# Performance work log

Measured on AMD Instinct MI355X. Metric: run time of the kernel, lower is better.

Reference implementation:

```python
import jax, jax.numpy as jnp
import numpy as np

B_, L_, H_, N_ = 8, 1024, 1024, 64

def setup_inputs() -> dict:
    key = jax.random.key(0)
    k1, k2, k3, k4 = jax.random.split(key, 4)
    return {
        "samples": jax.random.normal(k1, (B_, L_, 3 * H_), dtype=jnp.float32),
        "label_one_hot": jax.random.uniform(k2, (B_, L_, N_), dtype=jnp.float32),
        "predict": jax.random.normal(k3, (B_, L_, N_), dtype=jnp.float32),
        "W": jax.random.normal(k4, (H_, 3 * H_), dtype=jnp.float32) * (1.0 / np.sqrt(3 * H_)),
        "b_proj": jnp.zeros((H_,), dtype=jnp.float32),
    }

def reference(samples, label_one_hot, predict, W, b_proj):
    # projection: Linear(3H -> H)
    s = jnp.einsum("blk,hk->blh", samples, W) + b_proj          # [b,L,H]
    # dense similarity graph with diagonal masked out, row-softmax
    graph = jnp.einsum("blh,bmh->blm", s, s)                     # [b,L,L]
    L = graph.shape[1]
    eye = jnp.eye(L, dtype=graph.dtype)
    A = jax.nn.softmax(graph - 1e5 * eye, axis=-1)               # [b,L,L]
    # centered masked labels
    sup = label_one_hot
    row_has = (jnp.sum(sup, axis=-1) > 0.5).astype(sup.dtype)    # [b,L]
    total = jnp.sum(row_has, axis=-1)[:, None]                   # [b,1]
    avg = (jnp.sum(sup, axis=-2) / total)[:, None, :]            # [b,1,N]
    B0 = (sup - avg) * row_has[..., None]                        # [b,L,N]
    # diagonal inverse-degree scaling (elementwise, no dense diag matmul)
    d = 1.0 / (jnp.sum(A, axis=-1) + 1e-10)                      # [b,L]
    P = d[:, :, None] * jnp.swapaxes(A, -1, -2)                  # [b,L,L]
    Db = d[:, :, None] * B0                                      # [b,L,N]
    # 6-step power-iteration scan with residual injection at t==3
    ut = jnp.zeros_like(B0)
    for t in range(1, 7):
        ut = jnp.einsum("blm,bmn->bln", P, ut) + Db
        if t == 3:
            ut = ut + predict  # dropout is identity in eval mode
    return ut

if __name__ == "__main__":
    out = reference(**setup_inputs())
    print(out.shape, out.dtype)
```

## Files before the change

kernel.cpp:

```cpp
#include <hip/hip_runtime.h>


typedef _Float16 f16_t;
typedef f16_t f16x4 __attribute__((ext_vector_type(4)));
typedef f16_t f16x8 __attribute__((ext_vector_type(8)));
typedef float floatx4 __attribute__((ext_vector_type(4)));

__device__ __forceinline__ void async_copy16(const void* g, void* l) {
  __builtin_amdgcn_global_load_lds(
      (const __attribute__((address_space(1))) void*)g,
      (__attribute__((address_space(3))) void*)l, 16, 0, 0);
}

__device__ __forceinline__ f16_t hi_of(float x) { return (f16_t)x; }
__device__ __forceinline__ f16_t lo_of(float x, f16_t h) {
  return (f16_t)(x - (float)h);
}

__global__ __launch_bounds__(256) void prep_kernel(
    const float* __restrict__ W, f16_t* __restrict__ Whi, f16_t* __restrict__ Wlo,
    const float* __restrict__ samples, f16_t* __restrict__ SampH)
{
  const int bx = blockIdx.x, tid = threadIdx.x;
  if (bx < 3072) {
    const int i = bx * 256 + tid;
    float4 v = ((const float4*)W)[i];
    v.x *= 32.f; v.y *= 32.f; v.z *= 32.f; v.w *= 32.f;
    f16x4 h, l;
    f16_t h0 = hi_of(v.x); h[0] = h0; l[0] = lo_of(v.x, h0);
    f16_t h1 = hi_of(v.y); h[1] = h1; l[1] = lo_of(v.y, h1);
    f16_t h2 = hi_of(v.z); h[2] = h2; l[2] = lo_of(v.z, h2);
    f16_t h3 = hi_of(v.w); h[3] = h3; l[3] = lo_of(v.w, h3);
    *(f16x4*)(Whi + (size_t)i * 4) = h;
    *(f16x4*)(Wlo + (size_t)i * 4) = l;
  } else {
    const int i = (bx - 3072) * 256 + tid;
    const float4 v = ((const float4*)samples)[i];
    f16x4 h;
    h[0] = (f16_t)v.x; h[1] = (f16_t)v.y; h[2] = (f16_t)v.z; h[3] = (f16_t)v.w;
    *(f16x4*)(SampH + (size_t)i * 4) = h;
  }
}

struct Frags {
  f16x8 a[8];
  f16x8 bh0, bh1, bl0, bl1;
};

#define DSR(dst_, addr_, OFFSTR_) \
  asm volatile("ds_read_b128 %0, %1 offset:" OFFSTR_ : "=v"(dst_) : "v"(addr_))

__device__ __forceinline__ void read_frags_asm(unsigned sa, unsigned sb,
                                               Frags& f) {
  DSR(f.bh0, sb, "0");
  DSR(f.bh1, sb, "1024");
  DSR(f.bl0, sb, "8192");
  DSR(f.bl1, sb, "9216");
  DSR(f.a[0], sa, "0");
  DSR(f.a[1], sa, "1024");
  DSR(f.a[2], sa, "2048");
  DSR(f.a[3], sa, "3072");
  DSR(f.a[4], sa, "4096");
  DSR(f.a[5], sa, "5120");
  DSR(f.a[6], sa, "6144");
  DSR(f.a[7], sa, "7168");
}

__global__ __launch_bounds__(512, 2) void gemm1_pipe(
    const f16_t* __restrict__ Ag,
    const f16_t* __restrict__ BhG, const f16_t* __restrict__ BlG,
    const float* __restrict__ bias,
    f16_t* __restrict__ Chi, f16_t* __restrict__ Clo,
    int N, int K, float cscale)
{
  __shared__ __align__(16) char smem[131072];

  const int tid = threadIdx.x;
  const int lane = tid & 63;
  const int wave = tid >> 6;
  const int wm = wave >> 2;
  const int wn = wave & 3;
  const int bid0 = blockIdx.y * 8 + blockIdx.x;
  const int xk = bid0 & 7, xj = bid0 >> 3;
  const int m0 = ((xk >> 1) * 8 + (xj >> 2)) * 256;
  const int n0 = ((xk & 1) * 4 + (xj & 3)) * 128;
  const int fr = lane & 15;
  const int lch = lane >> 4;

  const int gA0 = tid;
  const int gA1 = tid + 512;
  const int rA0 = gA0 >> 2, lcA0 = (gA0 & 3) ^ ((rA0 >> 1) & 3);
  const int rA1 = gA1 >> 2, lcA1 = (gA1 & 3) ^ ((rA1 >> 1) & 3);
  const int rB = tid >> 2, lcB = (tid & 3) ^ ((rB >> 1) & 3);
  const f16_t* aSrc0 = Ag + (size_t)(m0 + rA0) * K + lcA0 * 8;
  const f16_t* aSrc1 = Ag + (size_t)(m0 + rA1) * K + lcA1 * 8;
  const f16_t* bhSrc = BhG + (size_t)(n0 + rB) * K + lcB * 8;
  const f16_t* blSrc = BlG + (size_t)(n0 + rB) * K + lcB * 8;
  char* ldsA0 = smem + gA0 * 16;
  char* ldsA1 = smem + gA1 * 16;
  char* ldsBh = smem + 16384 + (size_t)tid * 16;
  char* ldsBl = smem + 24576 + (size_t)tid * 16;

  const int swz = (lch ^ ((fr >> 1) & 3)) * 16;
  const int aoff = (wm * 128 + fr) * 64 + swz;
  const int boff = (wn * 32 + fr) * 64 + swz;
  const unsigned ldsBase =
      (unsigned)(size_t)(__attribute__((address_space(3))) char*)smem;
  const unsigned aA0 = ldsBase + (unsigned)aoff;
  const unsigned aA1 = aA0 + 32768u;
  const unsigned aA2 = aA0 + 65536u;
  const unsigned aA3 = aA0 + 98304u;
  const unsigned bA0 = ldsBase + 16384u + (unsigned)boff;
  const unsigned bA1 = bA0 + 32768u;
  const unsigned bA2 = bA0 + 65536u;
  const unsigned bA3 = bA0 + 98304u;

  floatx4 acc[8][2] = {};
  const int NS = K >> 5;

#define STAGE(SS_, SLOT_)                                     \
  do {                                                        \
    int ss = (SS_); if (ss >= NS) ss -= NS;                   \
    const int k0 = ss * 32;                                   \
    async_copy16(aSrc0 + k0, ldsA0 + (SLOT_) * 32768);        \
    async_copy16(aSrc1 + k0, ldsA1 + (SLOT_) * 32768);        \
    async_copy16(bhSrc + k0, ldsBh + (SLOT_) * 32768);        \
    async_copy16(blSrc + k0, ldsBl + (SLOT_) * 32768);        \
  } while (0)

#define MFMA8(F_, P_)                                                                                               \
  do {                                                                                                              \
    acc[2*(P_)][0]   = __builtin_amdgcn_mfma_f32_16x16x32_f16((F_).a[2*(P_)],   (F_).bh0, acc[2*(P_)][0],   0,0,0); \
    acc[2*(P_)][1]   = __builtin_amdgcn_mfma_f32_16x16x32_f16((F_).a[2*(P_)],   (F_).bh1, acc[2*(P_)][1],   0,0,0); \
    acc[2*(P_)+1][0] = __builtin_amdgcn_mfma_f32_16x16x32_f16((F_).a[2*(P_)+1], (F_).bh0, acc[2*(P_)+1][0], 0,0,0); \
    acc[2*(P_)+1][1] = __builtin_amdgcn_mfma_f32_16x16x32_f16((F_).a[2*(P_)+1], (F_).bh1, acc[2*(P_)+1][1], 0,0,0); \
    acc[2*(P_)][0]   = __builtin_amdgcn_mfma_f32_16x16x32_f16((F_).a[2*(P_)],   (F_).bl0, acc[2*(P_)][0],   0,0,0); \
    acc[2*(P_)][1]   = __builtin_amdgcn_mfma_f32_16x16x32_f16((F_).a[2*(P_)],   (F_).bl1, acc[2*(P_)][1],   0,0,0); \
    acc[2*(P_)+1][0] = __builtin_amdgcn_mfma_f32_16x16x32_f16((F_).a[2*(P_)+1], (F_).bl0, acc[2*(P_)+1][0], 0,0,0); \
    acc[2*(P_)+1][1] = __builtin_amdgcn_mfma_f32_16x16x32_f16((F_).a[2*(P_)+1], (F_).bl1, acc[2*(P_)+1][1], 0,0,0); \
  } while (0)

#define SB0 __builtin_amdgcn_sched_barrier(0)

#define HALF(SPRE_, SLOTPRE_, ARD_, BRD_, FRD_, FMM_)            \
  do {                                                           \
    STAGE(SPRE_, SLOTPRE_);                                      \
    asm volatile("s_waitcnt vmcnt(8)" ::: "memory");             \
    __builtin_amdgcn_s_barrier();                                \
    DSR(FRD_.bh0, BRD_, "0");                                    \
    DSR(FRD_.bh1, BRD_, "1024");                                 \
    DSR(FRD_.bl0, BRD_, "8192");                                 \
    SB0;                                                         \
    asm volatile("s_waitcnt lgkmcnt(3)" ::: "memory");           \
    SB0;                                                         \
    __builtin_amdgcn_s_setprio(1);                               \
    MFMA8(FMM_, 0);                                              \
    __builtin_amdgcn_s_setprio(0);                               \
    SB0;                                                         \
    DSR(FRD_.bl1, BRD_, "9216");                                 \
    DSR(FRD_.a[0], ARD_, "0");                                   \
    DSR(FRD_.a[1], ARD_, "1024");                                \
    SB0;                                                         \
    __builtin_amdgcn_s_setprio(1);                               \
    MFMA8(FMM_, 1);                                              \
    __builtin_amdgcn_s_setprio(0);                               \
    SB0;                                                         \
    DSR(FRD_.a[2], ARD_, "2048");                                \
    DSR(FRD_.a[3], ARD_, "3072");                                \
    DSR(FRD_.a[4], ARD_, "4096");                                \
    SB0;                                                         \
    __builtin_amdgcn_s_setprio(1);                               \
    MFMA8(FMM_, 2);                                              \
    __builtin_amdgcn_s_setprio(0);                               \
    SB0;                                                         \
    DSR(FRD_.a[5], ARD_, "5120");                                \
    DSR(FRD_.a[6], ARD_, "6144");                                \
    DSR(FRD_.a[7], ARD_, "7168");                                \
    SB0;                                                         \
    __builtin_amdgcn_s_setprio(1);                               \
    MFMA8(FMM_, 3);                                              \
    __builtin_amdgcn_s_setprio(0);                               \
    SB0;                                                         \
  } while (0)

  Frags f0, f1;

  STAGE(0, 0); STAGE(1, 1); STAGE(2, 2);
  asm volatile("s_waitcnt vmcnt(8)" ::: "memory");
  __builtin_amdgcn_s_barrier();
  read_frags_asm(aA0, bA0, f0);
  SB0;

  for (int s = 0; s < NS; s += 4) {
    HALF(s + 3, 3, aA1, bA1, f1, f0);
    HALF(s + 4, 0, aA2, bA2, f0, f1);
    HALF(s + 5, 1, aA3, bA3, f1, f0);
    HALF(s + 6, 2, aA0, bA0, f0, f1);
  }
  asm volatile("s_waitcnt vmcnt(0)" ::: "memory");
#undef HALF
#undef STAGE
#undef MFMA8

  const int mr = (lane >> 4) * 4;
#pragma unroll
  for (int j = 0; j < 2; ++j) {
    const int n = n0 + wn * 32 + j * 16 + fr;
    const float bj = bias[n];
#pragma unroll
    for (int i = 0; i < 8; ++i) {
#pragma unroll
      for (int r = 0; r < 4; ++r) {
        const int m = m0 + wm * 128 + i * 16 + mr + r;
        float v = acc[i][j][r] * cscale + bj;
        f16_t h = hi_of(v);
        Chi[(size_t)m * N + n] = h;
        Clo[(size_t)m * N + n] = lo_of(v, h);
      }
    }
  }
}

struct Frags2 {
  f16x8 a[4];
  f16x8 bh[4];
  f16x8 bl[4];
};

__global__ __launch_bounds__(256, 1) void gemm2_pipe(
    const f16_t* __restrict__ Sh, const f16_t* __restrict__ Sl,
    float* __restrict__ Gf)
{
  const int K = 1024, N = 1024;
  const long long bo = (long long)blockIdx.z * (1024LL * 1024);
  const f16_t* Ahi = Sh + bo;
  const f16_t* Bhi = Sh + bo;
  const f16_t* Blo = Sl + bo;
  float* Cf = Gf + bo;

  __shared__ __align__(16) char smem[98304];

  const int tid = threadIdx.x;
  const int lane = tid & 63;
  const int wave = tid >> 6;
  const int wm = wave >> 1, wn = wave & 1;

  int idx = blockIdx.x, ti = 0, accu = 0;
  while (accu + ti + 1 <= idx) { accu += ti + 1; ++ti; }
  const int m0 = ti * 128;
  const int n0 = (idx - accu) * 128;

  const int fr = lane & 15;
  const int lch = lane >> 4;

  const int gA0 = tid, gA1 = tid + 256;
  const int rA0 = gA0 >> 2, cA0 = (gA0 & 3) ^ ((rA0 >> 1) & 3);
  const int rA1 = gA1 >> 2, cA1 = (gA1 & 3) ^ ((rA1 >> 1) & 3);
  const f16_t* aSr0 = Ahi + (size_t)(m0 + rA0) * K + cA0 * 8;
  const f16_t* aSr1 = Ahi + (size_t)(m0 + rA1) * K + cA1 * 8;
  const f16_t* hSr0 = Bhi + (size_t)(n0 + rA0) * K + cA0 * 8;
  const f16_t* hSr1 = Bhi + (size_t)(n0 + rA1) * K + cA1 * 8;
  const f16_t* lSr0 = Blo + (size_t)(n0 + rA0) * K + cA0 * 8;
  const f16_t* lSr1 = Blo + (size_t)(n0 + rA1) * K + cA1 * 8;
  char* dA0 = smem + gA0 * 16;
  char* dA1 = smem + gA1 * 16;
  char* dH0 = smem + 8192 + gA0 * 16;
  char* dH1 = smem + 8192 + gA1 * 16;
  char* dL0 = smem + 16384 + gA0 * 16;
  char* dL1 = smem + 16384 + gA1 * 16;

  const int swz16 = (lch ^ ((fr >> 1) & 3)) * 16;
  const int aoff = (wm * 64 + fr) * 64 + swz16;
  const int boff = (wn * 64 + fr) * 64 + swz16;
  const unsigned ldsBase =
      (unsigned)(size_t)(__attribute__((address_space(3))) char*)smem;
  const unsigned aS0 = ldsBase + (unsigned)aoff;
  const unsigned aS1 = aS0 + 24576u;
  const unsigned aS2 = aS0 + 49152u;
  const unsigned aS3 = aS0 + 73728u;
  const unsigned bS0 = ldsBase + 8192u + (unsigned)boff;
  const unsigned bS1 = bS0 + 24576u;
  const unsigned bS2 = bS0 + 49152u;
  const unsigned bS3 = bS0 + 73728u;

  floatx4 acc[4][4] = {};
  const int NS = 32;

#define STAGE2(SS_, SLOT_)                                    \
  do {                                                        \
    int ss = (SS_); if (ss >= NS) ss -= NS;                   \
    const int k0 = ss * 32;                                   \
    async_copy16(aSr0 + k0, dA0 + (SLOT_) * 24576);           \
    async_copy16(aSr1 + k0, dA1 + (SLOT_) * 24576);           \
    async_copy16(hSr0 + k0, dH0 + (SLOT_) * 24576);           \
    async_copy16(hSr1 + k0, dH1 + (SLOT_) * 24576);           \
    async_copy16(lSr0 + k0, dL0 + (SLOT_) * 24576);           \
    async_copy16(lSr1 + k0, dL1 + (SLOT_) * 24576);           \
  } while (0)

#define MFMA8_2(F_, P_)                                                                              \
  do {                                                                                               \
    acc[0][P_] = __builtin_amdgcn_mfma_f32_16x16x32_f16((F_).a[0], (F_).bh[P_], acc[0][P_], 0,0,0);  \
    acc[1][P_] = __builtin_amdgcn_mfma_f32_16x16x32_f16((F_).a[1], (F_).bh[P_], acc[1][P_], 0,0,0);  \
    acc[2][P_] = __builtin_amdgcn_mfma_f32_16x16x32_f16((F_).a[2], (F_).bh[P_], acc[2][P_], 0,0,0);  \
    acc[3][P_] = __builtin_amdgcn_mfma_f32_16x16x32_f16((F_).a[3], (F_).bh[P_], acc[3][P_], 0,0,0);  \
    acc[0][P_] = __builtin_amdgcn_mfma_f32_16x16x32_f16((F_).a[0], (F_).bl[P_], acc[0][P_], 0,0,0);  \
    acc[1][P_] = __builtin_amdgcn_mfma_f32_16x16x32_f16((F_).a[1], (F_).bl[P_], acc[1][P_], 0,0,0);  \
    acc[2][P_] = __builtin_amdgcn_mfma_f32_16x16x32_f16((F_).a[2], (F_).bl[P_], acc[2][P_], 0,0,0);  \
    acc[3][P_] = __builtin_amdgcn_mfma_f32_16x16x32_f16((F_).a[3], (F_).bl[P_], acc[3][P_], 0,0,0);  \
  } while (0)

#define SB0 __builtin_amdgcn_sched_barrier(0)

#define GR2(SPRE_, SLOTPRE_, ARD_, BRD_, FRD_, FMM_)             \
  do {                                                           \
    STAGE2(SPRE_, SLOTPRE_);                                     \
    asm volatile("s_waitcnt vmcnt(12)" ::: "memory");            \
    __builtin_amdgcn_s_barrier();                                \
    DSR(FRD_.bh[0], BRD_, "0");                                  \
    DSR(FRD_.bh[1], BRD_, "1024");                               \
    DSR(FRD_.bh[2], BRD_, "2048");                               \
    SB0;                                                         \
    asm volatile("s_waitcnt lgkmcnt(3)" ::: "memory");           \
    SB0;                                                         \
    __builtin_amdgcn_s_setprio(1);                               \
    MFMA8_2(FMM_, 0);                                            \
    __builtin_amdgcn_s_setprio(0);                               \
    SB0;                                                         \
    DSR(FRD_.bh[3], BRD_, "3072");                               \
    DSR(FRD_.bl[0], BRD_, "8192");                               \
    DSR(FRD_.bl[1], BRD_, "9216");                               \
    SB0;                                                         \
    __builtin_amdgcn_s_setprio(1);                               \
    MFMA8_2(FMM_, 1);                                            \
    __builtin_amdgcn_s_setprio(0);                               \
    SB0;                                                         \
    DSR(FRD_.bl[2], BRD_, "10240");                              \
    DSR(FRD_.bl[3], BRD_, "11264");                              \
    DSR(FRD_.a[0], ARD_, "0");                                   \
    SB0;                                                         \
    __builtin_amdgcn_s_setprio(1);                               \
    MFMA8_2(FMM_, 2);                                            \
    __builtin_amdgcn_s_setprio(0);                               \
    SB0;                                                         \
    DSR(FRD_.a[1], ARD_, "1024");                                \
    DSR(FRD_.a[2], ARD_, "2048");                                \
    DSR(FRD_.a[3], ARD_, "3072");                                \
    SB0;                                                         \
    __builtin_amdgcn_s_setprio(1);                               \
    MFMA8_2(FMM_, 3);                                            \
    __builtin_amdgcn_s_setprio(0);                               \
    SB0;                                                         \
  } while (0)

  Frags2 f0, f1;

  STAGE2(0, 0); STAGE2(1, 1); STAGE2(2, 2);
  asm volatile("s_waitcnt vmcnt(12)" ::: "memory");
  __builtin_amdgcn_s_barrier();
  DSR(f0.bh[0], bS0, "0");
  DSR(f0.bh[1], bS0, "1024");
  DSR(f0.bh[2], bS0, "2048");
  DSR(f0.bh[3], bS0, "3072");
  DSR(f0.bl[0], bS0, "8192");
  DSR(f0.bl[1], bS0, "9216");
  DSR(f0.bl[2], bS0, "10240");
  DSR(f0.bl[3], bS0, "11264");
  DSR(f0.a[0], aS0, "0");
  DSR(f0.a[1], aS0, "1024");
  DSR(f0.a[2], aS0, "2048");
  DSR(f0.a[3], aS0, "3072");
  SB0;

  for (int s = 0; s < NS; s += 4) {
    GR2(s + 3, 3, aS1, bS1, f1, f0);
    GR2(s + 4, 0, aS2, bS2, f0, f1);
    GR2(s + 5, 1, aS3, bS3, f1, f0);
    GR2(s + 6, 2, aS0, bS0, f0, f1);
  }
  asm volatile("s_waitcnt vmcnt(0)" ::: "memory");
#undef GR2
#undef MFMA8_2
#undef STAGE2

  const int mr = (lane >> 4) * 4;
#pragma unroll
  for (int j = 0; j < 4; ++j) {
    const int n = n0 + wn * 64 + j * 16 + fr;
#pragma unroll
    for (int i = 0; i < 4; ++i) {
#pragma unroll
      for (int r = 0; r < 4; ++r) {
        const int m = m0 + wm * 64 + i * 16 + mr + r;
        float v = acc[i][j][r];
        if (m == n) v -= 1e5f;
        Cf[(size_t)m * N + n] = v;
      }
    }
  }

  if (m0 != n0) {
    float* T = (float*)smem;
#pragma unroll
    for (int mc = 0; mc < 4; ++mc) {
      __syncthreads();
      if (wm == (mc >> 1)) {
        const int ibase = (mc & 1) * 2;
#pragma unroll
        for (int di = 0; di < 2; ++di) {
#pragma unroll
          for (int j = 0; j < 4; ++j) {
            const int nl = wn * 64 + j * 16 + fr;
#pragma unroll
            for (int r = 0; r < 4; ++r) {
              const int mloc = di * 16 + mr + r;
              T[nl * 36 + mloc] = acc[ibase + di][j][r];
            }
          }
        }
      }
      __syncthreads();
      const int row = tid >> 1, half = tid & 1;
      const float* src = &T[row * 36 + half * 16];
      float* dst = Cf + (size_t)(n0 + row) * N + m0 + mc * 32 + half * 16;
#pragma unroll
      for (int q = 0; q < 16; ++q) dst[q] = src[q];
    }
  }
}

__global__ __launch_bounds__(256) void rowstats_kernel(
    const float* __restrict__ G, float* __restrict__ mx, float* __restrict__ inv)
{
  __shared__ float red[4];
  const int tid = threadIdx.x;
  const float* g = G + (size_t)blockIdx.x * 1024;
  const float4 v = ((const float4*)g)[tid];

  float m = fmaxf(fmaxf(v.x, v.y), fmaxf(v.z, v.w));
#pragma unroll
  for (int off = 32; off > 0; off >>= 1) m = fmaxf(m, __shfl_down(m, off));
  if ((tid & 63) == 0) red[tid >> 6] = m;
  __syncthreads();
  m = fmaxf(fmaxf(red[0], red[1]), fmaxf(red[2], red[3]));
  __syncthreads();

  float s = __expf(v.x - m) + __expf(v.y - m) + __expf(v.z - m) + __expf(v.w - m);
#pragma unroll
  for (int off = 32; off > 0; off >>= 1) s += __shfl_down(s, off);
  if ((tid & 63) == 0) red[tid >> 6] = s;
  __syncthreads();
  if (tid == 0) {
    mx[blockIdx.x] = m;
    inv[blockIdx.x] = 1.0f / (red[0] + red[1] + red[2] + red[3]);
  }
}

__global__ __launch_bounds__(256) void make_at_kernel(
    const float* __restrict__ G, const float* __restrict__ mx,
    const float* __restrict__ inv, f16_t* __restrict__ At)
{
  const int row = blockIdx.x;
  const int b = row >> 10;
  const int tid = threadIdx.x;
  const float4 g = ((const float4*)(G + (size_t)row * 1024))[tid];
  const float4 m = ((const float4*)(mx + b * 1024))[tid];
  const float4 iv = ((const float4*)(inv + b * 1024))[tid];
  f16x4 o;
  o[0] = (f16_t)(__expf(g.x - m.x) * iv.x);
  o[1] = (f16_t)(__expf(g.y - m.y) * iv.y);
  o[2] = (f16_t)(__expf(g.z - m.z) * iv.z);
  o[3] = (f16_t)(__expf(g.w - m.w) * iv.w);
  *(f16x4*)(At + (size_t)row * 1024 + tid * 4) = o;
}

__global__ __launch_bounds__(1024) void make_db_kernel(
    const float* __restrict__ sup, float* __restrict__ Db, f16_t* __restrict__ DbT)
{
  const int L = 1024, Nn = 64;
  const float* s = sup + (size_t)blockIdx.x * L * Nn;
  float* db = Db + (size_t)blockIdx.x * L * Nn;
  f16_t* dbt = DbT + (size_t)blockIdx.x * L * Nn;
  __shared__ float rowhas[1024];
  __shared__ float cpart[1024];
  __shared__ float tpart[16];
  __shared__ float avg[64];
  __shared__ float totalsh;
  const int tid = threadIdx.x;

  const float4* sr = (const float4*)(s + (size_t)tid * 64);
  float ss = 0.f;
#pragma unroll
  for (int i = 0; i < 16; ++i) { const float4 v = sr[i]; ss += (v.x + v.y) + (v.z + v.w); }
  const float rh = (ss > 0.5f) ? 1.f : 0.f;
  rowhas[tid] = rh;
  float t = rh;
#pragma unroll
  for (int off = 32; off > 0; off >>= 1) t += __shfl_down(t, off);
  if ((tid & 63) == 0) tpart[tid >> 6] = t;

  const int n = tid & 63, seg = tid >> 6;
  float cs = 0.f;
  for (int l = seg * 64; l < seg * 64 + 64; ++l) cs += s[(size_t)l * 64 + n];
  cpart[seg * 64 + n] = cs;
  __syncthreads();
  if (tid == 0) { float tt = 0.f; for (int i = 0; i < 16; ++i) tt += tpart[i]; totalsh = tt; }
  __syncthreads();
  if (tid < 64) {
    float a = 0.f;
    for (int i = 0; i < 16; ++i) a += cpart[i * 64 + tid];
    avg[tid] = a / totalsh;
  }
  __syncthreads();

  const float4* s4 = (const float4*)s;
  float4* d4 = (float4*)db;
  for (int i = tid; i < (L * Nn) / 4; i += 1024) {
    float4 v = s4[i];
    const int l = i >> 4;
    const int nb = (i & 15) * 4;
    const float rhl = rowhas[l];
    v.x = (v.x - avg[nb + 0]) * rhl;
    v.y = (v.y - avg[nb + 1]) * rhl;
    v.z = (v.z - avg[nb + 2]) * rhl;
    v.w = (v.w - avg[nb + 3]) * rhl;
    d4[i] = v;
  }
  for (int i = tid; i < L * Nn; i += 1024) {
    const int n2 = i >> 10, l2 = i & 1023;
    dbt[i] = (f16_t)((s[(size_t)l2 * 64 + n2] - avg[n2]) * rowhas[l2]);
  }
}

template <int PRED, int FINAL>
__global__ __launch_bounds__(256) void iter_step(
    const f16_t* __restrict__ At, const f16_t* __restrict__ UT,
    const float* __restrict__ Db, const float* __restrict__ Pred,
    f16_t* __restrict__ UTn, float* __restrict__ OutF)
{
  const int L = 1024, Nn = 64;
  const int b = blockIdx.y, l0 = blockIdx.x * 32;
  At += (size_t)b * L * L;
  UT += (size_t)b * Nn * L;

  __shared__ __align__(16) char smem[131072];

  const int tid = threadIdx.x;
  const int lane = tid & 63;
  const int wave = tid >> 6;
  const int fr = lane & 15;
  const int lch = lane >> 4;
  const int mwb = wave * 256;

  int g_, rw_, sc_;
  g_ = lane;        rw_ = g_ >> 3; sc_ = (g_ & 7) ^ (rw_ & 7);
  const f16_t* aS0 = At + (size_t)(l0 + rw_) * L + mwb + sc_ * 8;
  g_ = lane + 64;   rw_ = g_ >> 3; sc_ = (g_ & 7) ^ (rw_ & 7);
  const f16_t* aS1 = At + (size_t)(l0 + rw_) * L + mwb + sc_ * 8;
  g_ = lane + 128;  rw_ = g_ >> 3; sc_ = (g_ & 7) ^ (rw_ & 7);
  const f16_t* aS2 = At + (size_t)(l0 + rw_) * L + mwb + sc_ * 8;
  g_ = lane + 192;  rw_ = g_ >> 3; sc_ = (g_ & 7) ^ (rw_ & 7);
  const f16_t* aS3 = At + (size_t)(l0 + rw_) * L + mwb + sc_ * 8;
  g_ = lane;        rw_ = g_ >> 3; sc_ = (g_ & 7) ^ (rw_ & 7);
  const f16_t* uS0 = UT + (size_t)rw_ * L + mwb + sc_ * 8;
  g_ = lane + 64;   rw_ = g_ >> 3; sc_ = (g_ & 7) ^ (rw_ & 7);
  const f16_t* uS1 = UT + (size_t)rw_ * L + mwb + sc_ * 8;
  g_ = lane + 128;  rw_ = g_ >> 3; sc_ = (g_ & 7) ^ (rw_ & 7);
  const f16_t* uS2 = UT + (size_t)rw_ * L + mwb + sc_ * 8;
  g_ = lane + 192;  rw_ = g_ >> 3; sc_ = (g_ & 7) ^ (rw_ & 7);
  const f16_t* uS3 = UT + (size_t)rw_ * L + mwb + sc_ * 8;
  g_ = lane + 256;  rw_ = g_ >> 3; sc_ = (g_ & 7) ^ (rw_ & 7);
  const f16_t* uS4 = UT + (size_t)rw_ * L + mwb + sc_ * 8;
  g_ = lane + 320;  rw_ = g_ >> 3; sc_ = (g_ & 7) ^ (rw_ & 7);
  const f16_t* uS5 = UT + (size_t)rw_ * L + mwb + sc_ * 8;
  g_ = lane + 384;  rw_ = g_ >> 3; sc_ = (g_ & 7) ^ (rw_ & 7);
  const f16_t* uS6 = UT + (size_t)rw_ * L + mwb + sc_ * 8;
  g_ = lane + 448;  rw_ = g_ >> 3; sc_ = (g_ & 7) ^ (rw_ & 7);
  const f16_t* uS7 = UT + (size_t)rw_ * L + mwb + sc_ * 8;

  char* stA = smem + wave * 24576;
  char* stU = stA + 4096;

  const int offK0 = fr * 128 + ((lch ^ (fr & 7)) * 16);
  const int offK1 = fr * 128 + (((4 + lch) ^ (fr & 7)) * 16);

  floatx4 acc[2][4] = {};

#define STG(M0_, BUF_)                                        \
  do {                                                        \
    char* dA = stA + (BUF_) * 12288;                          \
    char* dU = stU + (BUF_) * 12288;                          \
    async_copy16(aS0 + (M0_), dA + lane * 16);                \
    async_copy16(aS1 + (M0_), dA + 1024 + lane * 16);         \
    async_copy16(aS2 + (M0_), dA + 2048 + lane * 16);         \
    async_copy16(aS3 + (M0_), dA + 3072 + lane * 16);         \
    async_copy16(uS0 + (M0_), dU + lane * 16);                \
    async_copy16(uS1 + (M0_), dU + 1024 + lane * 16);         \
    async_copy16(uS2 + (M0_), dU + 2048 + lane * 16);         \
    async_copy16(uS3 + (M0_), dU + 3072 + lane * 16);         \
    async_copy16(uS4 + (M0_), dU + 4096 + lane * 16);         \
    async_copy16(uS5 + (M0_), dU + 5120 + lane * 16);         \
    async_copy16(uS6 + (M0_), dU + 6144 + lane * 16);         \
    async_copy16(uS7 + (M0_), dU + 7168 + lane * 16);         \
  } while (0)

#define LD8(b_, o_) (*(const f16x8*)((b_) + (o_)))
#define MM(A_, U_, C_) C_ = __builtin_amdgcn_mfma_f32_16x16x32_f16(A_, U_, C_, 0, 0, 0)

#define CHUNK(BUF_)                                                       \
  do {                                                                    \
    const char* cA = stA + (BUF_) * 12288;                                \
    const char* cU = stU + (BUF_) * 12288;                                \
    f16x8 a00 = LD8(cA, offK0), a01 = LD8(cA, offK1);                     \
    f16x8 a10 = LD8(cA, offK0 + 2048), a11 = LD8(cA, offK1 + 2048);       \
    f16x8 u00 = LD8(cU, offK0), u01 = LD8(cU, offK1);                     \
    f16x8 u10 = LD8(cU, offK0 + 2048), u11 = LD8(cU, offK1 + 2048);       \
    f16x8 u20 = LD8(cU, offK0 + 4096), u21 = LD8(cU, offK1 + 4096);       \
    f16x8 u30 = LD8(cU, offK0 + 6144), u31 = LD8(cU, offK1 + 6144);       \
    MM(a00, u00, acc[0][0]); MM(a00, u10, acc[0][1]);                     \
    MM(a00, u20, acc[0][2]); MM(a00, u30, acc[0][3]);                     \
    MM(a10, u00, acc[1][0]); MM(a10, u10, acc[1][1]);                     \
    MM(a10, u20, acc[1][2]); MM(a10, u30, acc[1][3]);                     \
    MM(a01, u01, acc[0][0]); MM(a01, u11, acc[0][1]);                     \
    MM(a01, u21, acc[0][2]); MM(a01, u31, acc[0][3]);                     \
    MM(a11, u01, acc[1][0]); MM(a11, u11, acc[1][1]);                     \
    MM(a11, u21, acc[1][2]); MM(a11, u31, acc[1][3]);                     \
  } while (0)

#define SB0 __builtin_amdgcn_sched_barrier(0)

  STG(0, 0);
  STG(64, 1);
  asm volatile("s_waitcnt vmcnt(12)" ::: "memory");
  SB0;
  CHUNK(0);
  SB0;
  STG(128, 0);
  asm volatile("s_waitcnt vmcnt(12)" ::: "memory");
  SB0;
  CHUNK(1);
  SB0;
  STG(192, 1);
  asm volatile("s_waitcnt vmcnt(12)" ::: "memory");
  SB0;
  CHUNK(0);
  SB0;
  asm volatile("s_waitcnt vmcnt(0)" ::: "memory");
  SB0;
  CHUNK(1);
#undef CHUNK
#undef STG

  float* P = (float*)(smem + 98304) + wave * 2048;
  const int mr = (lane >> 4) * 4;
#pragma unroll
  for (int li = 0; li < 2; ++li)
#pragma unroll
    for (int j = 0; j < 4; ++j)
#pragma unroll
      for (int r = 0; r < 4; ++r)
        P[(li * 16 + mr + r) * 64 + j * 16 + fr] = acc[li][j][r];
  __syncthreads();

  const float* P0 = (const float*)(smem + 98304);
  const size_t obase = ((size_t)b * L + l0) * Nn;
  f16_t* OutS = (f16_t*)smem;
#pragma unroll
  for (int it = 0; it < 2; ++it) {
    const int e4 = it * 256 + tid;
    const int l = e4 >> 4, n4 = (e4 & 15) * 4;
    const int eo = l * 64 + n4;
    float4 v = *(const float4*)(P0 + eo);
    const float4 p1 = *(const float4*)(P0 + 2048 + eo);
    const float4 p2 = *(const float4*)(P0 + 4096 + eo);
    const float4 p3 = *(const float4*)(P0 + 6144 + eo);
    v.x += p1.x; v.y += p1.y; v.z += p1.z; v.w += p1.w;
    v.x += p2.x; v.y += p2.y; v.z += p2.z; v.w += p2.w;
    v.x += p3.x; v.y += p3.y; v.z += p3.z; v.w += p3.w;
    const float4 d = *(const float4*)(Db + obase + eo);
    v.x += d.x; v.y += d.y; v.z += d.z; v.w += d.w;
    if (PRED) {
      const float4 p = *(const float4*)(Pred + obase + eo);
      v.x += p.x; v.y += p.y; v.z += p.z; v.w += p.w;
    }
    if (FINAL) {
      *(float4*)(OutF + obase + eo) = v;
    } else {
      OutS[(n4 + 0) * 40 + l] = (f16_t)v.x;
      OutS[(n4 + 1) * 40 + l] = (f16_t)v.y;
      OutS[(n4 + 2) * 40 + l] = (f16_t)v.z;
      OutS[(n4 + 3) * 40 + l] = (f16_t)v.w;
    }
  }
  if (!FINAL) {
    __syncthreads();
    f16_t* dst = UTn + (size_t)b * Nn * L + l0;
    const int n = tid >> 2, lc = (tid & 3) * 8;
    *(f16x8*)(dst + (size_t)n * L + lc) = *(const f16x8*)&OutS[n * 40 + lc];
  }
#undef SB0
#undef LD8
#undef MM
}

extern "C" void kernel_launch(void* const* d_in, const int* in_sizes, int n_in,
                              void* d_out, int out_size, void* d_ws, size_t ws_size,
                              hipStream_t stream) {
  const float* samples = (const float*)d_in[0];
  const float* label   = (const float*)d_in[1];
  const float* predict = (const float*)d_in[2];
  const float* W       = (const float*)d_in[3];
  const float* bproj   = (const float*)d_in[4];
  float* out = (float*)d_out;

  char* ws = (char*)d_ws;
  f16_t* Whi = (f16_t*)ws;
  f16_t* Wlo = (f16_t*)(ws + 6291456);
  float* mx  = (float*)ws;
  float* inv = (float*)(ws + 32768);
  float* Db  = (float*)(ws + 65536);
  f16_t* DbT = (f16_t*)(ws + 65536 + 2097152);
  f16_t* UTa = (f16_t*)(ws + 65536 + 3145728);
  f16_t* UTb = (f16_t*)(ws + 65536 + 4194304);
  f16_t* SampH = (f16_t*)(ws + 12582912);
  float* G     = (float*)(ws + 12582912);
  f16_t* Shi = (f16_t*)(ws + 62914560);
  f16_t* Slo = (f16_t*)(ws + 62914560 + 16777216);
  f16_t* At  = Shi;

  prep_kernel<<<dim3(27648), 256, 0, stream>>>(W, Whi, Wlo, samples, SampH);

  gemm1_pipe<<<dim3(8, 32), 512, 0, stream>>>(
      SampH, Whi, Wlo, bproj, Shi, Slo, 1024, 3072, 1.0f / 32.0f);

  gemm2_pipe<<<dim3(36, 1, 8), 256, 0, stream>>>(Shi, Slo, G);

  rowstats_kernel<<<8192, 256, 0, stream>>>(G, mx, inv);
  make_at_kernel<<<8192, 256, 0, stream>>>(G, mx, inv, At);

  make_db_kernel<<<8, 1024, 0, stream>>>(label, Db, DbT);

  dim3 gi(32, 8);
  iter_step<0, 0><<<gi, 256, 0, stream>>>(At, DbT, Db, nullptr, UTa, nullptr);
  iter_step<1, 0><<<gi, 256, 0, stream>>>(At, UTa, Db, predict, UTb, nullptr);
  iter_step<0, 0><<<gi, 256, 0, stream>>>(At, UTb, Db, nullptr, UTa, nullptr);
  iter_step<0, 0><<<gi, 256, 0, stream>>>(At, UTa, Db, nullptr, UTb, nullptr);
  iter_step<0, 1><<<gi, 256, 0, stream>>>(At, UTb, Db, nullptr, nullptr, out);
}
```

Baseline: 382.0 us.

## Shrink gemm2 pipeline to three stages, batch rowstats rows, parallelize Db prep

The gemm2 LDS ring drops from four stages to three, using 72KB instead of 96KB, so two blocks can share a CU under the new launch bound; the loop is restructured with an explicit epilogue. The rowstats and make_at kernels now handle four rows per block, which cuts block count and launch overhead. The single-block-per-batch make_db kernel becomes two kernels over 128 blocks: one computes partial column and row stats, the other applies them and writes a coalesced transpose through LDS. The risks are a shallower prefetch pipeline in gemm2 and register pressure from the occupancy-2 bound.

Result: faster. 353.8 us (-7.4%).

```diff
diff --git a/kernel.cpp b/kernel.cpp
--- a/kernel.cpp
+++ b/kernel.cpp
@@ -227,7 +227,7 @@
   f16x8 bl[4];
 };
 
-__global__ __launch_bounds__(256, 1) void gemm2_pipe(
+__global__ __launch_bounds__(256, 2) void gemm2_pipe(
     const f16_t* __restrict__ Sh, const f16_t* __restrict__ Sl,
     float* __restrict__ Gf)
 {
@@ -238,7 +238,7 @@
   const f16_t* Blo = Sl + bo;
   float* Cf = Gf + bo;
 
-  __shared__ __align__(16) char smem[98304];
+  __shared__ __align__(16) char smem[73728];
 
   const int tid = threadIdx.x;
   const int lane = tid & 63;
@@ -274,14 +274,12 @@
   const int boff = (wn * 64 + fr) * 64 + swz16;
   const unsigned ldsBase =
       (unsigned)(size_t)(__attribute__((address_space(3))) char*)smem;
-  const unsigned aS0 = ldsBase + (unsigned)aoff;
-  const unsigned aS1 = aS0 + 24576u;
-  const unsigned aS2 = aS0 + 49152u;
-  const unsigned aS3 = aS0 + 73728u;
-  const unsigned bS0 = ldsBase + 8192u + (unsigned)boff;
-  const unsigned bS1 = bS0 + 24576u;
-  const unsigned bS2 = bS0 + 49152u;
-  const unsigned bS3 = bS0 + 73728u;
+  const unsigned aT0 = ldsBase + (unsigned)aoff;
+  const unsigned aT1 = aT0 + 24576u;
+  const unsigned aT2 = aT0 + 49152u;
+  const unsigned bT0 = ldsBase + 8192u + (unsigned)boff;
+  const unsigned bT1 = bT0 + 24576u;
+  const unsigned bT2 = bT0 + 49152u;
 
   floatx4 acc[4][4] = {};
   const int NS = 32;
@@ -312,10 +310,10 @@
 
 #define SB0 __builtin_amdgcn_sched_barrier(0)
 
-#define GR2(SPRE_, SLOTPRE_, ARD_, BRD_, FRD_, FMM_)             \
+#define GR3(SPRE_, SLOTPRE_, ARD_, BRD_, FRD_, FMM_)             \
   do {                                                           \
     STAGE2(SPRE_, SLOTPRE_);                                     \
-    asm volatile("s_waitcnt vmcnt(12)" ::: "memory");            \
+    asm volatile("s_waitcnt vmcnt(6)" ::: "memory");             \
     __builtin_amdgcn_s_barrier();                                \
     DSR(FRD_.bh[0], BRD_, "0");                                  \
     DSR(FRD_.bh[1], BRD_, "1024");                               \
@@ -355,31 +353,58 @@
 
   Frags2 f0, f1;
 
-  STAGE2(0, 0); STAGE2(1, 1); STAGE2(2, 2);
-  asm volatile("s_waitcnt vmcnt(12)" ::: "memory");
+  STAGE2(0, 0); STAGE2(1, 1);
+  asm volatile("s_waitcnt vmcnt(6)" ::: "memory");
   __builtin_amdgcn_s_barrier();
-  DSR(f0.bh[0], bS0, "0");
-  DSR(f0.bh[1], bS0, "1024");
-  DSR(f0.bh[2], bS0, "2048");
-  DSR(f0.bh[3], bS0, "3072");
-  DSR(f0.bl[0], bS0, "8192");
-  DSR(f0.bl[1], bS0, "9216");
-  DSR(f0.bl[2], bS0, "10240");
-  DSR(f0.bl[3], bS0, "11264");
-  DSR(f0.a[0], aS0, "0");
-  DSR(f0.a[1], aS0, "1024");
-  DSR(f0.a[2], aS0, "2048");
-  DSR(f0.a[3], aS0, "3072");
-  SB0;
-
-  for (int s = 0; s < NS; s += 4) {
-    GR2(s + 3, 3, aS1, bS1, f1, f0);
-    GR2(s + 4, 0, aS2, bS2, f0, f1);
-    GR2(s + 5, 1, aS3, bS3, f1, f0);
-    GR2(s + 6, 2, aS0, bS0, f0, f1);
+  DSR(f0.bh[0], bT0, "0");
+  DSR(f0.bh[1], bT0, "1024");
+  DSR(f0.bh[2], bT0, "2048");
+  DSR(f0.bh[3], bT0, "3072");
+  DSR(f0.bl[0], bT0, "8192");
+  DSR(f0.bl[1], bT0, "9216");
+  DSR(f0.bl[2], bT0, "10240");
+  DSR(f0.bl[3], bT0, "11264");
+  DSR(f0.a[0], aT0, "0");
+  DSR(f0.a[1], aT0, "1024");
+  DSR(f0.a[2], aT0, "2048");
+  DSR(f0.a[3], aT0, "3072");
+  SB0;
+
+  for (int s = 0; s < 30; s += 6) {
+    GR3(s + 2, 2, aT1, bT1, f1, f0);
+    GR3(s + 3, 0, aT2, bT2, f0, f1);
+    GR3(s + 4, 1, aT0, bT0, f1, f0);
+    GR3(s + 5, 2, aT1, bT1, f0, f1);
+    GR3(s + 6, 0, aT2, bT2, f1, f0);
+    GR3(s + 7, 1, aT0, bT0, f0, f1);
   }
   asm volatile("s_waitcnt vmcnt(0)" ::: "memory");
-#undef GR2
+  __builtin_amdgcn_s_barrier();
+  DSR(f1.bh[0], bT1, "0");
+  DSR(f1.bh[1], bT1, "1024");
+  DSR(f1.bh[2], bT1, "2048");
+  DSR(f1.bh[3], bT1, "3072");
+  DSR(f1.bl[0], bT1, "8192");
+  DSR(f1.bl[1], bT1, "9216");
+  DSR(f1.bl[2], bT1, "10240");
+  DSR(f1.bl[3], bT1, "11264");
+  DSR(f1.a[0], aT1, "0");
+  DSR(f1.a[1], aT1, "1024");
+  DSR(f1.a[2], aT1, "2048");
+  DSR(f1.a[3], aT1, "3072");
+  SB0;
+  asm volatile("s_waitcnt lgkmcnt(12)" ::: "memory");
+  SB0;
+  __builtin_amdgcn_s_setprio(1);
+  MFMA8_2(f0, 0); MFMA8_2(f0, 1); MFMA8_2(f0, 2); MFMA8_2(f0, 3);
+  __builtin_amdgcn_s_setprio(0);
+  SB0;
+  asm volatile("s_waitcnt lgkmcnt(0)" ::: "memory");
+  SB0;
+  __builtin_amdgcn_s_setprio(1);
+  MFMA8_2(f1, 0); MFMA8_2(f1, 1); MFMA8_2(f1, 2); MFMA8_2(f1, 3);
+  __builtin_amdgcn_s_setprio(0);
+#undef GR3
 #undef MFMA8_2
 #undef STAGE2
 
@@ -432,27 +457,57 @@
 __global__ __launch_bounds__(256) void rowstats_kernel(
     const float* __restrict__ G, float* __restrict__ mx, float* __restrict__ inv)
 {
-  __shared__ float red[4];
+  __shared__ float redm[4][4], reds[4][4], mxsh[4];
   const int tid = threadIdx.x;
-  const float* g = G + (size_t)blockIdx.x * 1024;
-  const float4 v = ((const float4*)g)[tid];
-
-  float m = fmaxf(fmaxf(v.x, v.y), fmaxf(v.z, v.w));
-#pragma unroll
-  for (int off = 32; off > 0; off >>= 1) m = fmaxf(m, __shfl_down(m, off));
-  if ((tid & 63) == 0) red[tid >> 6] = m;
+  const int r0 = blockIdx.x * 4;
+  const float* g = G + (size_t)r0 * 1024;
+  const float4 v0 = ((const float4*)g)[tid];
+  const float4 v1 = ((const float4*)(g + 1024))[tid];
+  const float4 v2 = ((const float4*)(g + 2048))[tid];
+  const float4 v3 = ((const float4*)(g + 3072))[tid];
+
+  float m0 = fmaxf(fmaxf(v0.x, v0.y), fmaxf(v0.z, v0.w));
+  float m1 = fmaxf(fmaxf(v1.x, v1.y), fmaxf(v1.z, v1.w));
+  float m2 = fmaxf(fmaxf(v2.x, v2.y), fmaxf(v2.z, v2.w));
+  float m3 = fmaxf(fmaxf(v3.x, v3.y), fmaxf(v3.z, v3.w));
+#pragma unroll
+  for (int off = 32; off > 0; off >>= 1) {
+    m0 = fmaxf(m0, __shfl_down(m0, off));
+    m1 = fmaxf(m1, __shfl_down(m1, off));
+    m2 = fmaxf(m2, __shfl_down(m2, off));
+    m3 = fmaxf(m3, __shfl_down(m3, off));
+  }
+  if ((tid & 63) == 0) {
+    redm[0][tid >> 6] = m0; redm[1][tid >> 6] = m1;
+    redm[2][tid >> 6] = m2; redm[3][tid >> 6] = m3;
+  }
   __syncthreads();
-  m = fmaxf(fmaxf(red[0], red[1]), fmaxf(red[2], red[3]));
+  if (tid < 4)
+    mxsh[tid] = fmaxf(fmaxf(redm[tid][0], redm[tid][1]),
+                      fmaxf(redm[tid][2], redm[tid][3]));
   __syncthreads();
-
-  float s = __expf(v.x - m) + __expf(v.y - m) + __expf(v.z - m) + __expf(v.w - m);
-#pragma unroll
-  for (int off = 32; off > 0; off >>= 1) s += __shfl_down(s, off);
-  if ((tid & 63) == 0) red[tid >> 6] = s;
+  const float M0 = mxsh[0], M1 = mxsh[1], M2 = mxsh[2], M3 = mxsh[3];
+
+  float s0 = __expf(v0.x - M0) + __expf(v0.y - M0) + __expf(v0.z - M0) + __expf(v0.w - M0);
+  float s1 = __expf(v1.x - M1) + __expf(v1.y - M1) + __expf(v1.z - M1) + __expf(v1.w - M1);
+  float s2 = __expf(v2.x - M2) + __expf(v2.y - M2) + __expf(v2.z - M2) + __expf(v2.w - M2);
+  float s3 = __expf(v3.x - M3) + __expf(v3.y - M3) + __expf(v3.z - M3) + __expf(v3.w - M3);
+#pragma unroll
+  for (int off = 32; off > 0; off >>= 1) {
+    s0 += __shfl_down(s0, off);
+    s1 += __shfl_down(s1, off);
+    s2 += __shfl_down(s2, off);
+    s3 += __shfl_down(s3, off);
+  }
+  if ((tid & 63) == 0) {
+    reds[0][tid >> 6] = s0; reds[1][tid >> 6] = s1;
+    reds[2][tid >> 6] = s2; reds[3][tid >> 6] = s3;
+  }
   __syncthreads();
-  if (tid == 0) {
-    mx[blockIdx.x] = m;
-    inv[blockIdx.x] = 1.0f / (red[0] + red[1] + red[2] + red[3]);
+  if (tid < 4) {
+    mx[r0 + tid] = mxsh[tid];
+    inv[r0 + tid] = 1.0f /
+        (reds[tid][0] + reds[tid][1] + reds[tid][2] + reds[tid][3]);
   }
 }
 
@@ -460,76 +515,134 @@
     const float* __restrict__ G, const float* __restrict__ mx,
     const float* __restrict__ inv, f16_t* __restrict__ At)
 {
-  const int row = blockIdx.x;
-  const int b = row >> 10;
+  const int r0 = blockIdx.x * 4;
+  const int b = r0 >> 10;
   const int tid = threadIdx.x;
-  const float4 g = ((const float4*)(G + (size_t)row * 1024))[tid];
   const float4 m = ((const float4*)(mx + b * 1024))[tid];
   const float4 iv = ((const float4*)(inv + b * 1024))[tid];
-  f16x4 o;
-  o[0] = (f16_t)(__expf(g.x - m.x) * iv.x);
-  o[1] = (f16_t)(__expf(g.y - m.y) * iv.y);
-  o[2] = (f16_t)(__expf(g.z - m.z) * iv.z);
-  o[3] = (f16_t)(__expf(g.w - m.w) * iv.w);
-  *(f16x4*)(At + (size_t)row * 1024 + tid * 4) = o;
-}
-
-__global__ __launch_bounds__(1024) void make_db_kernel(
-    const float* __restrict__ sup, float* __restrict__ Db, f16_t* __restrict__ DbT)
+#pragma unroll
+  for (int k = 0; k < 4; ++k) {
+    const float4 g = ((const float4*)(G + (size_t)(r0 + k) * 1024))[tid];
+    f16x4 o;
+    o[0] = (f16_t)(__expf(g.x - m.x) * iv.x);
+    o[1] = (f16_t)(__expf(g.y - m.y) * iv.y);
+    o[2] = (f16_t)(__expf(g.z - m.z) * iv.z);
+    o[3] = (f16_t)(__expf(g.w - m.w) * iv.w);
+    *(f16x4*)(At + (size_t)(r0 + k) * 1024 + tid * 4) = o;
+  }
+}
+
+__global__ __launch_bounds__(256) void db_stats(
+    const float* __restrict__ sup, float* __restrict__ colpart,
+    float* __restrict__ totalpart)
 {
-  const int L = 1024, Nn = 64;
-  const float* s = sup + (size_t)blockIdx.x * L * Nn;
-  float* db = Db + (size_t)blockIdx.x * L * Nn;
-  f16_t* dbt = DbT + (size_t)blockIdx.x * L * Nn;
-  __shared__ float rowhas[1024];
-  __shared__ float cpart[1024];
-  __shared__ float tpart[16];
-  __shared__ float avg[64];
-  __shared__ float totalsh;
+  const int b = blockIdx.x >> 4, chunk = blockIdx.x & 15;
   const int tid = threadIdx.x;
-
-  const float4* sr = (const float4*)(s + (size_t)tid * 64);
-  float ss = 0.f;
-#pragma unroll
-  for (int i = 0; i < 16; ++i) { const float4 v = sr[i]; ss += (v.x + v.y) + (v.z + v.w); }
-  const float rh = (ss > 0.5f) ? 1.f : 0.f;
-  rowhas[tid] = rh;
-  float t = rh;
-#pragma unroll
-  for (int off = 32; off > 0; off >>= 1) t += __shfl_down(t, off);
-  if ((tid & 63) == 0) tpart[tid >> 6] = t;
-
-  const int n = tid & 63, seg = tid >> 6;
-  float cs = 0.f;
-  for (int l = seg * 64; l < seg * 64 + 64; ++l) cs += s[(size_t)l * 64 + n];
-  cpart[seg * 64 + n] = cs;
+  const int r = tid >> 2, q = tid & 3;
+  const float* s = sup + ((size_t)b * 1024 + chunk * 64 + r) * 64 + q * 16;
+  const float4 x0 = ((const float4*)s)[0];
+  const float4 x1 = ((const float4*)s)[1];
+  const float4 x2 = ((const float4*)s)[2];
+  const float4 x3 = ((const float4*)s)[3];
+
+  float rs = (x0.x + x0.y + x0.z + x0.w) + (x1.x + x1.y + x1.z + x1.w) +
+             (x2.x + x2.y + x2.z + x2.w) + (x3.x + x3.y + x3.z + x3.w);
+  rs += __shfl_xor(rs, 1);
+  rs += __shfl_xor(rs, 2);
+  const float rh = (rs > 0.5f) ? 1.f : 0.f;
+
+  __shared__ float colp[64];
+  __shared__ float tp[4];
+  if (tid < 64) colp[tid] = 0.f;
   __syncthreads();
-  if (tid == 0) { float tt = 0.f; for (int i = 0; i < 16; ++i) tt += tpart[i]; totalsh = tt; }
+  atomicAdd(&colp[q * 16 + 0], x0.x);  atomicAdd(&colp[q * 16 + 1], x0.y);
+  atomicAdd(&colp[q * 16 + 2], x0.z);  atomicAdd(&colp[q * 16 + 3], x0.w);
+  atomicAdd(&colp[q * 16 + 4], x1.x);  atomicAdd(&colp[q * 16 + 5], x1.y);
+  atomicAdd(&colp[q * 16 + 6], x1.z);  atomicAdd(&colp[q * 16 + 7], x1.w);
+  atomicAdd(&colp[q * 16 + 8], x2.x);  atomicAdd(&colp[q * 16 + 9], x2.y);
+  atomicAdd(&colp[q * 16 + 10], x2.z); atomicAdd(&colp[q * 16 + 11], x2.w);
+  atomicAdd(&colp[q * 16 + 12], x3.x); atomicAdd(&colp[q * 16 + 13], x3.y);
+  atomicAdd(&colp[q * 16 + 14], x3.z); atomicAdd(&colp[q * 16 + 15], x3.w);
+
+  float ts = (q == 0) ? rh : 0.f;
+#pragma unroll
+  for (int off = 32; off > 0; off >>= 1) ts += __shfl_down(ts, off);
+  if ((tid & 63) == 0) tp[tid >> 6] = ts;
   __syncthreads();
+  if (tid < 64) colpart[((size_t)b * 16 + chunk) * 64 + tid] = colp[tid];
+  if (tid == 0) totalpart[b * 16 + chunk] = tp[0] + tp[1] + tp[2] + tp[3];
+}
+
+__global__ __launch_bounds__(256) void db_apply(
+    const float* __restrict__ sup, const float* __restrict__ colpart,
+    const float* __restrict__ totalpart,
+    float* __restrict__ Db, f16_t* __restrict__ DbT)
+{
+  const int b = blockIdx.x >> 4, chunk = blockIdx.x & 15;
+  const int tid = threadIdx.x;
+  const int r = tid >> 2, q = tid & 3;
+
+  __shared__ float avgsh[64];
+  __shared__ float totsh;
+  __shared__ f16_t DbTs[64 * 72];
+
+  float a = 0.f;
   if (tid < 64) {
-    float a = 0.f;
-    for (int i = 0; i < 16; ++i) a += cpart[i * 64 + tid];
-    avg[tid] = a / totalsh;
+#pragma unroll
+    for (int c = 0; c < 16; ++c) a += colpart[((size_t)b * 16 + c) * 64 + tid];
+  }
+  if (tid == 0) {
+    float tt = 0.f;
+#pragma unroll
+    for (int c = 0; c < 16; ++c) tt += totalpart[b * 16 + c];
+    totsh = tt;
   }
   __syncthreads();
-
-  const float4* s4 = (const float4*)s;
-  float4* d4 = (float4*)db;
-  for (int i = tid; i < (L * Nn) / 4; i += 1024) {
-    float4 v = s4[i];
-    const int l = i >> 4;
-    const int nb = (i & 15) * 4;
-    const float rhl = rowhas[l];
-    v.x = (v.x - avg[nb + 0]) * rhl;
-    v.y = (v.y - avg[nb + 1]) * rhl;
-    v.z = (v.z - avg[nb + 2]) * rhl;
-    v.w = (v.w - avg[nb + 3]) * rhl;
-    d4[i] = v;
-  }
-  for (int i = tid; i < L * Nn; i += 1024) {
-    const int n2 = i >> 10, l2 = i & 1023;
-    dbt[i] = (f16_t)((s[(size_t)l2 * 64 + n2] - avg[n2]) * rowhas[l2]);
-  }
+  if (tid < 64) avgsh[tid] = a / totsh;
+  __syncthreads();
+
+  const size_t rowoff = ((size_t)b * 1024 + chunk * 64 + r) * 64 + q * 16;
+  const float* s = sup + rowoff;
+  float4 x0 = ((const float4*)s)[0];
+  float4 x1 = ((const float4*)s)[1];
+  float4 x2 = ((const float4*)s)[2];
+  float4 x3 = ((const float4*)s)[3];
+
+  float rs = (x0.x + x0.y + x0.z + x0.w) + (x1.x + x1.y + x1.z + x1.w) +
+             (x2.x + x2.y + x2.z + x2.w) + (x3.x + x3.y + x3.z + x3.w);
+  rs += __shfl_xor(rs, 1);
+  rs += __shfl_xor(rs, 2);
+  const float rh = (rs > 0.5f) ? 1.f : 0.f;
+
+  const int nb = q * 16;
+  x0.x = (x0.x - avgsh[nb + 0]) * rh;  x0.y = (x0.y - avgsh[nb + 1]) * rh;
+  x0.z = (x0.z - avgsh[nb + 2]) * rh;  x0.w = (x0.w - avgsh[nb + 3]) * rh;
+  x1.x = (x1.x - avgsh[nb + 4]) * rh;  x1.y = (x1.y - avgsh[nb + 5]) * rh;
+  x1.z = (x1.z - avgsh[nb + 6]) * rh;  x1.w = (x1.w - avgsh[nb + 7]) * rh;
+  x2.x = (x2.x - avgsh[nb + 8]) * rh;  x2.y = (x2.y - avgsh[nb + 9]) * rh;
+  x2.z = (x2.z - avgsh[nb + 10]) * rh; x2.w = (x2.w - avgsh[nb + 11]) * rh;
+  x3.x = (x3.x - avgsh[nb + 12]) * rh; x3.y = (x3.y - avgsh[nb + 13]) * rh;
+  x3.z = (x3.z - avgsh[nb + 14]) * rh; x3.w = (x3.w - avgsh[nb + 15]) * rh;
+
+  float* d = Db + rowoff;
+  ((float4*)d)[0] = x0; ((float4*)d)[1] = x1;
+  ((float4*)d)[2] = x2; ((float4*)d)[3] = x3;
+
+  DbTs[(nb + 0) * 72 + r] = (f16_t)x0.x;  DbTs[(nb + 1) * 72 + r] = (f16_t)x0.y;
+  DbTs[(nb + 2) * 72 + r] = (f16_t)x0.z;  DbTs[(nb + 3) * 72 + r] = (f16_t)x0.w;
+  DbTs[(nb + 4) * 72 + r] = (f16_t)x1.x;  DbTs[(nb + 5) * 72 + r] = (f16_t)x1.y;
+  DbTs[(nb + 6) * 72 + r] = (f16_t)x1.z;  DbTs[(nb + 7) * 72 + r] = (f16_t)x1.w;
+  DbTs[(nb + 8) * 72 + r] = (f16_t)x2.x;  DbTs[(nb + 9) * 72 + r] = (f16_t)x2.y;
+  DbTs[(nb + 10) * 72 + r] = (f16_t)x2.z; DbTs[(nb + 11) * 72 + r] = (f16_t)x2.w;
+  DbTs[(nb + 12) * 72 + r] = (f16_t)x3.x; DbTs[(nb + 13) * 72 + r] = (f16_t)x3.y;
+  DbTs[(nb + 14) * 72 + r] = (f16_t)x3.z; DbTs[(nb + 15) * 72 + r] = (f16_t)x3.w;
+  __syncthreads();
+
+  const int n = tid >> 2, seg = tid & 3;
+  const f16_t* src = &DbTs[n * 72 + seg * 16];
+  f16_t* dst = DbT + ((size_t)b * 64 + n) * 1024 + chunk * 64 + seg * 16;
+  *(f16x8*)dst = *(const f16x8*)src;
+  *(f16x8*)(dst + 8) = *(const f16x8*)(src + 8);
 }
 
 template <int PRED, int FINAL>
@@ -722,6 +835,8 @@
   f16_t* DbT = (f16_t*)(ws + 65536 + 2097152);
   f16_t* UTa = (f16_t*)(ws + 65536 + 3145728);
   f16_t* UTb = (f16_t*)(ws + 65536 + 4194304);
+  float* colpart   = (float*)(ws + 5308416);
+  float* totalpart = (float*)(ws + 5308416 + 32768);
   f16_t* SampH = (f16_t*)(ws + 12582912);
   float* G     = (float*)(ws + 12582912);
   f16_t* Shi = (f16_t*)(ws + 62914560);
@@ -735,10 +850,11 @@
 
   gemm2_pipe<<<dim3(36, 1, 8), 256, 0, stream>>>(Shi, Slo, G);
 
-  rowstats_kernel<<<8192, 256, 0, stream>>>(G, mx, inv);
-  make_at_kernel<<<8192, 256, 0, stream>>>(G, mx, inv, At);
-
-  make_db_kernel<<<8, 1024, 0, stream>>>(label, Db, DbT);
+  rowstats_kernel<<<2048, 256, 0, stream>>>(G, mx, inv);
+  make_at_kernel<<<2048, 256, 0, stream>>>(G, mx, inv, At);
+
+  db_stats<<<128, 256, 0, stream>>>(label, colpart, totalpart);
+  db_apply<<<128, 256, 0, stream>>>(label, colpart, totalpart, Db, DbT);
 
   dim3 gi(32, 8);
   iter_step<0, 0><<<gi, 256, 0, stream>>>(At, DbT, Db, nullptr, UTa, nullptr);
```
